# Performance work log

Measured on AMD Instinct MI355X. Metric: run time of the kernel, lower is better.

The kernel has to match this reference:

```python
import jax, jax.numpy as jnp
import numpy as np

N_NODES = 100000
N_EDGES = 1600000
D_IN = 128
D_HID = 128


def gcn_conv(x, src, dst, deg_inv_sqrt, W, b, n_nodes):
    """GCNConv: out = D^{-1/2}(A+I)D^{-1/2} (x @ W) + b.

    src/dst already include self-loops; deg_inv_sqrt precomputed per node.
    """
    h = x @ W  # [N, D_out]
    coef = deg_inv_sqrt[src] * deg_inv_sqrt[dst]  # [E+N]
    msg = h[src] * coef[:, None]  # [E+N, D_out] -- dominant memory traffic
    out = jax.ops.segment_sum(msg, dst, num_segments=n_nodes)
    return out + b


def reference(x, edge_index, W1, b1, W2, b2):
    n_nodes = x.shape[0]
    loop = jnp.arange(n_nodes, dtype=edge_index.dtype)
    src = jnp.concatenate([edge_index[0], loop])
    dst = jnp.concatenate([edge_index[1], loop])
    deg = jax.ops.segment_sum(jnp.ones_like(src, dtype=x.dtype), dst,
                              num_segments=n_nodes)
    deg_inv_sqrt = jnp.where(deg > 0, jax.lax.rsqrt(jnp.maximum(deg, 1.0)), 0.0)

    h = gcn_conv(x, src, dst, deg_inv_sqrt, W1, b1, n_nodes)
    h = jax.nn.relu(h)
    h = gcn_conv(h, src, dst, deg_inv_sqrt, W2, b2, n_nodes)
    return h.mean(axis=0)  # [D_HID]


def setup_inputs() -> dict:
    key = jax.random.key(0)
    k1, k2, k3, k4, k5 = jax.random.split(key, 5)
    x = jax.random.normal(k1, (N_NODES, D_IN), dtype=jnp.float32)
    edge_index = jax.random.randint(k2, (2, N_EDGES), 0, N_NODES, dtype=jnp.int64)
    s1 = 1.0 / np.sqrt(D_IN)
    s2 = 1.0 / np.sqrt(D_HID)
    W1 = jax.random.uniform(k3, (D_IN, D_HID), jnp.float32, -s1, s1)
    W2 = jax.random.uniform(k4, (D_HID, D_HID), jnp.float32, -s2, s2)
    b1 = jnp.zeros((D_HID,), jnp.float32)
    b2 = jnp.zeros((D_HID,), jnp.float32)
    return {"x": x, "edge_index": edge_index, "W1": W1, "b1": b1,
            "W2": W2, "b2": b2}
```

## Files before the change

### kernel.cpp

```cpp
#include <hip/hip_runtime.h>

#define NN 100000
#define NE 1600000
#define DD 128
#define BSH 8
#define NB 391
#define CAP 4608
#define CAPP 8704
#define SSH 9
#define NBS 196
#define CAP2 9472
#define NAB 6250
#define NRB 125

typedef float f32x2 __attribute__((ext_vector_type(2)));
typedef float f32x4 __attribute__((ext_vector_type(4)));
typedef short s16x8 __attribute__((ext_vector_type(8)));

static __device__ __forceinline__ unsigned short f2bf(float f) {
    unsigned u = __float_as_uint(f);
    return (unsigned short)((u + 0x7fffu + ((u >> 16) & 1u)) >> 16);
}


__global__ __launch_bounds__(256) void k_part(const int* __restrict__ src, const int* __restrict__ dst,
                                              int* __restrict__ bcursor, int* __restrict__ bcursor2,
                                              unsigned* __restrict__ part, unsigned* __restrict__ part2) {
    __shared__ int histD[NB], rankD[NB], bblD[NB];
    __shared__ int histS[NBS], rankS[NBS], bblS[NBS];
    int t = threadIdx.x;
    for (int j = t; j < NB; j += 256) histD[j] = 0;
    if (t < NBS) histS[t] = 0;
    __syncthreads();
    int base = blockIdx.x * 4096;
    int s[16], d[16];
    #pragma unroll
    for (int j = 0; j < 16; j++) {
        int i = base + j * 256 + t;
        if (i < NE) {
            s[j] = src[i]; d[j] = dst[i];
            atomicAdd(&histD[d[j] >> BSH], 1);
            atomicAdd(&histS[s[j] >> SSH], 1);
        } else d[j] = -1;
    }
    __syncthreads();
    for (int j = t; j < NB; j += 256) { bblD[j] = atomicAdd(&bcursor[j], histD[j]);  rankD[j] = 0; }
    if (t < NBS) { bblS[t] = atomicAdd(&bcursor2[t], histS[t]); rankS[t] = 0; }
    __syncthreads();
    #pragma unroll
    for (int j = 0; j < 16; j++) {
        if (d[j] >= 0) {
            int bD = d[j] >> BSH;
            int r = bblD[bD] + atomicAdd(&rankD[bD], 1);
            if (r < CAP)
                part[(size_t)bD * CAP + r] = (unsigned)s[j] | ((unsigned)(d[j] & 255) << 17);
            int bS = s[j] >> SSH;
            int r2 = bblS[bS] + atomicAdd(&rankS[bS], 1);
            if (r2 < CAP2)
                part2[(size_t)bS * CAP2 + r2] = (unsigned)d[j] | ((unsigned)(s[j] & 511) << 17);
        }
    }
}


__global__ __launch_bounds__(256) void k_csr(const unsigned* __restrict__ part, const int* __restrict__ bcursor,
                                             int* __restrict__ offs, int* __restrict__ oend,
                                             float* __restrict__ dis, int* __restrict__ csr,
                                             unsigned* __restrict__ hs) {
    __shared__ int cnt[256], offl[256], s2[256];
    int t = threadIdx.x;
    int b = blockIdx.x;
    if (b == 0 && t < 32) hs[(unsigned)NN * 32u + t] = 0u;
    int dlo = b << BSH;
    int nn_b = NN - dlo; if (nn_b > 256) nn_b = 256;
    int c = bcursor[b]; if (c > CAP) c = CAP;
    size_t e0 = (size_t)b * CAP;
    int e0p = b * CAPP;
    cnt[t] = 0;
    __syncthreads();
    for (int i = t; i < c; i += 256)
        atomicAdd(&cnt[part[e0 + i] >> 17], 1);
    __syncthreads();
    int a = cnt[t];
    int ap = (a + 15) & ~15;
    s2[t] = ap;
    __syncthreads();
    for (int off = 1; off < 256; off <<= 1) {
        int add = (t >= off) ? s2[t - off] : 0;
        __syncthreads();
        s2[t] += add;
        __syncthreads();
    }
    int ex = s2[t] - ap;
    offl[t] = ex;
    if (t < nn_b) {
        offs[dlo + t] = e0p + ex;
        oend[dlo + t] = e0p + ex + ap;
        dis[dlo + t] = rsqrtf((float)a + 1.0f);
    }
    cnt[t] = 0;
    __syncthreads();
    for (int i = t; i < c; i += 256) {
        unsigned e = part[e0 + i];
        int li = (int)(e >> 17);
        int p = e0p + offl[li] + atomicAdd(&cnt[li], 1);
        csr[p] = (int)(e & 0x1FFFFu);
    }
    __syncthreads();
    if (t < nn_b) {
        int base2 = e0p + offl[t];
        for (int i = a; i < ap; i++) csr[base2 + i] = NN;
    }
}


__global__ __launch_bounds__(256) void k_coefb(const unsigned* __restrict__ part2, const int* __restrict__ bcursor2,
                                               const float* __restrict__ dis, float* __restrict__ coef) {
    __shared__ float accL[512];
    int t = threadIdx.x;
    int b = blockIdx.x;
    int dlo = b << SSH;
    int nn_b = NN - dlo; if (nn_b > 512) nn_b = 512;
    int c = bcursor2[b]; if (c > CAP2) c = CAP2;
    size_t e0 = (size_t)b * CAP2;
    accL[t] = 0.f; accL[t + 256] = 0.f;
    __syncthreads();
    for (int i = t; i < c; i += 256) {
        unsigned e = part2[e0 + i];
        atomicAdd(&accL[e >> 17], dis[e & 0x1FFFFu]);
    }
    __syncthreads();
    #pragma unroll
    for (int q = 0; q < 2; q++) {
        int i = t + q * 256;
        if (i < nn_b) coef[dlo + i] = accL[i];
    }
}


__global__ __launch_bounds__(256) void k_gemm(const float* __restrict__ Ap, const float* __restrict__ W,
                                              const float* __restrict__ dis, unsigned* __restrict__ hs) {
    __shared__ unsigned WF[8192];
    int tid = threadIdx.x;
    #pragma unroll
    for (int i = 0; i < 32; i++) {
        int e = i * 256 + tid;
        int jw = e & 3, lane = (e >> 2) & 63, kk = (e >> 8) & 3, nt = e >> 10;
        int r0 = kk * 32 + ((lane >> 4) << 3) + (jw << 1);
        int c = (nt << 4) + (lane & 15);
        unsigned lo = f2bf(W[r0 * DD + c]);
        unsigned hi = f2bf(W[(r0 + 1) * DD + c]);
        WF[e] = lo | (hi << 16);
    }

    int lane = tid & 63;
    int w = tid >> 6;
    int rowBase = blockIdx.x * 128 + w * 32;
    int lg = lane >> 4;
    int ll = lane & 15;

    s16x8 af[2][4];
    #pragma unroll
    for (int mt = 0; mt < 2; mt++) {
        int r = rowBase + mt * 16 + ll;
        if (r >= NN) r = NN - 1;
        const char* xp = (const char*)Ap + ((unsigned)r * 512u + (unsigned)lg * 32u);
        #pragma unroll
        for (int kk = 0; kk < 4; kk++) {
            f32x4 a0 = *(const f32x4*)(xp + kk * 128);
            f32x4 a1 = *(const f32x4*)(xp + kk * 128 + 16);
            s16x8 tt;
            tt[0] = (short)f2bf(a0[0]); tt[1] = (short)f2bf(a0[1]);
            tt[2] = (short)f2bf(a0[2]); tt[3] = (short)f2bf(a0[3]);
            tt[4] = (short)f2bf(a1[0]); tt[5] = (short)f2bf(a1[1]);
            tt[6] = (short)f2bf(a1[2]); tt[7] = (short)f2bf(a1[3]);
            af[mt][kk] = tt;
        }
    }
    __syncthreads();

    f32x4 acc[2][8];
    #pragma unroll
    for (int m = 0; m < 2; m++)
        #pragma unroll
        for (int n = 0; n < 8; n++) acc[m][n] = (f32x4){0.f, 0.f, 0.f, 0.f};

    const s16x8* wfrag = (const s16x8*)WF;

    #pragma unroll
    for (int kk = 0; kk < 4; kk++) {
        #pragma unroll
        for (int nt = 0; nt < 8; nt++) {
            s16x8 bf = wfrag[(nt * 4 + kk) * 64 + lane];
            acc[0][nt] = __builtin_amdgcn_mfma_f32_16x16x32_bf16(bf, af[0][kk], acc[0][nt], 0, 0, 0);
            acc[1][nt] = __builtin_amdgcn_mfma_f32_16x16x32_bf16(bf, af[1][kk], acc[1][nt], 0, 0, 0);
        }
    }

    #pragma unroll
    for (int mt = 0; mt < 2; mt++) {
        int grow = rowBase + mt * 16 + ll;
        if (grow < NN) {
            float dn = dis[grow];
            unsigned* orow = (unsigned*)((char*)hs + ((unsigned)grow * 128u));
            #pragma unroll
            for (int nt = 0; nt < 8; nt++) {
                f32x4 v = acc[mt][nt];
                int u = 0;
                u = __builtin_amdgcn_cvt_pk_fp8_f32(v[0] * dn, v[1] * dn, u, false);
                u = __builtin_amdgcn_cvt_pk_fp8_f32(v[2] * dn, v[3] * dn, u, true);
                orow[nt * 4 + lg] = (unsigned)u;
            }
        }
    }
}


__global__ __launch_bounds__(256) void k_agg1(const unsigned* __restrict__ hs4, const float* __restrict__ dis,
                                              const int* __restrict__ offs, const int* __restrict__ oend,
                                              const int* __restrict__ csr, const float* __restrict__ bias,
                                              const float* __restrict__ coef, float* __restrict__ partials) {
    __shared__ float red[4][DD];
    int lane = threadIdx.x & 63;
    int half = lane >> 5;
    int li = lane & 31;
    int wv = threadIdx.x >> 6;
    int node0 = (blockIdx.x * 4 + wv) * 4;
    unsigned li4 = (unsigned)li << 2;
    const char* hb = (const char*)hs4;
    f32x2 v01 = {0.f, 0.f}, v23 = {0.f, 0.f};
    f32x4 bv = *(const f32x4*)&bias[li * 4];

    #pragma unroll 1
    for (int q = 0; q < 4; q++) {
        int node = node0 + q;
        int beg = offs[node], endp = oend[node];
        float dn = dis[node];
        f32x2 a01 = {0.f, 0.f}, a23 = {0.f, 0.f};

        #pragma unroll 1
        for (int i = beg; i < endp; i += 16) {
            const int* cp = csr + i + half * 8;
            int4 sa = *(const int4*)cp;
            int4 sb = *(const int4*)(cp + 4);
            unsigned r[8];
            r[0] = *(const unsigned*)(hb + (((unsigned)sa.x << 7) + li4));
            r[1] = *(const unsigned*)(hb + (((unsigned)sa.y << 7) + li4));
            r[2] = *(const unsigned*)(hb + (((unsigned)sa.z << 7) + li4));
            r[3] = *(const unsigned*)(hb + (((unsigned)sa.w << 7) + li4));
            r[4] = *(const unsigned*)(hb + (((unsigned)sb.x << 7) + li4));
            r[5] = *(const unsigned*)(hb + (((unsigned)sb.y << 7) + li4));
            r[6] = *(const unsigned*)(hb + (((unsigned)sb.z << 7) + li4));
            r[7] = *(const unsigned*)(hb + (((unsigned)sb.w << 7) + li4));
            #pragma unroll
            for (int j = 0; j < 8; j++) {
                a01 += __builtin_amdgcn_cvt_pk_f32_fp8(r[j], false);
                a23 += __builtin_amdgcn_cvt_pk_f32_fp8(r[j], true);
            }
        }

        a01[0] += __shfl_xor(a01[0], 32);
        a01[1] += __shfl_xor(a01[1], 32);
        a23[0] += __shfl_xor(a23[0], 32);
        a23[1] += __shfl_xor(a23[1], 32);

        if (half == 0) {
            unsigned su = *(const unsigned*)(hb + (((unsigned)node << 7) + li4));
            f32x2 sl = __builtin_amdgcn_cvt_pk_f32_fp8(su, false);
            f32x2 sh = __builtin_amdgcn_cvt_pk_f32_fp8(su, true);
            float o0 = fmaxf(dn * (a01[0] + sl[0]) + bv[0], 0.f);
            float o1 = fmaxf(dn * (a01[1] + sl[1]) + bv[1], 0.f);
            float o2 = fmaxf(dn * (a23[0] + sh[0]) + bv[2], 0.f);
            float o3 = fmaxf(dn * (a23[1] + sh[1]) + bv[3], 0.f);
            float wt = (coef[node] + dn) * dn;
            v01[0] += wt * o0; v01[1] += wt * o1;
            v23[0] += wt * o2; v23[1] += wt * o3;
        }
    }

    if (half == 0) {
        red[wv][li * 4 + 0] = v01[0];
        red[wv][li * 4 + 1] = v01[1];
        red[wv][li * 4 + 2] = v23[0];
        red[wv][li * 4 + 3] = v23[1];
    }
    __syncthreads();
    int t = threadIdx.x;
    if (t < DD)
        partials[(size_t)blockIdx.x * DD + t] = red[0][t] + red[1][t] + red[2][t] + red[3][t];
}


__global__ __launch_bounds__(128) void k_red1(const float* __restrict__ partials, float* __restrict__ s1) {
    int t = threadIdx.x, b = blockIdx.x;
    float s = 0.f;
    for (int r = b * 50; r < b * 50 + 50; r++) s += partials[(size_t)r * DD + t];
    s1[b * DD + t] = s;
}

__global__ __launch_bounds__(128) void k_out(const float* __restrict__ s1, const float* __restrict__ W2,
                                             const float* __restrict__ b2, float* __restrict__ out) {
    __shared__ float v[DD];
    int t = threadIdx.x;
    float s = 0.f;
    for (int r = 0; r < NRB; r++) s += s1[r * DD + t];
    v[t] = s * (1.0f / NN);
    __syncthreads();
    float o = b2[t];
    for (int k = 0; k < DD; k++) o += v[k] * W2[k * DD + t];
    out[t] = o;
}


extern "C" void kernel_launch(void* const* d_in, const int* in_sizes, int n_in,
                              void* d_out, int out_size, void* d_ws, size_t ws_size,
                              hipStream_t stream) {
    const float* x  = (const float*)d_in[0];
    const int*   ei = (const int*)d_in[1];
    const float* W1 = (const float*)d_in[2];
    const float* b1 = (const float*)d_in[3];
    const float* W2 = (const float*)d_in[4];
    const float* b2 = (const float*)d_in[5];
    float* out = (float*)d_out;
    const int* esrc = ei;
    const int* edst = ei + NE;

    char* p = (char*)d_ws;
    unsigned* part  = (unsigned*)p;      p += (size_t)NB * CAP * 4;
    unsigned* part2 = (unsigned*)p;      p += (size_t)NBS * CAP2 * 4;
    int* csr       = (int*)p;            p += (size_t)NB * CAPP * 4;
    int* offs      = (int*)p;            p += (((size_t)NN * 4) + 255) & ~(size_t)255;
    int* oend      = (int*)p;            p += (((size_t)NN * 4) + 255) & ~(size_t)255;
    float* dis     = (float*)p;          p += (((size_t)NN * 4) + 255) & ~(size_t)255;
    float* coef    = (float*)p;          p += (((size_t)NN * 4) + 255) & ~(size_t)255;
    int* bcursor   = (int*)p;            p += (((size_t)(NB + NBS) * 4) + 255) & ~(size_t)255;
    unsigned* hs   = (unsigned*)p;       p += (size_t)(NN + 1) * DD;
    float* partials = (float*)p;         p += (size_t)NAB * DD * 4;
    float* s1      = (float*)p;          p += (size_t)NRB * DD * 4;
    int* bcursor2  = bcursor + NB;

    hipMemsetAsync(bcursor, 0, (NB + NBS) * 4, stream);

    k_part<<<(NE + 4095) / 4096, 256, 0, stream>>>(esrc, edst, bcursor, bcursor2, part, part2);
    k_csr<<<NB, 256, 0, stream>>>(part, bcursor, offs, oend, dis, csr, hs);
    k_coefb<<<NBS, 256, 0, stream>>>(part2, bcursor2, dis, coef);

    k_gemm<<<(NN + 127) / 128, 256, 0, stream>>>(x, W1, dis, hs);
    k_agg1<<<NAB, 256, 0, stream>>>(hs, dis, offs, oend, csr, b1, coef, partials);

    k_red1<<<NRB, 128, 0, stream>>>(partials, s1);
    k_out<<<1, 128, 0, stream>>>(s1, W2, b2, out);
}
```

Before: 153.2 us.

## Fuse coef kernel into GEMM launch and prefetch next CSR indices in aggregation

The separate coefficient-accumulation kernel is merged into the GEMM kernel as extra blocks that branch off by block index and reuse the GEMM's shared buffer. This removes one kernel launch and lets the small coef work run alongside the GEMM blocks. The aggregation loop now loads the next 16 CSR indices before issuing the current gathers, a software prefetch meant to hide index-load latency. That prefetch reads past each node's end, so the CSR buffer is padded by 16 ints; the fused kernel also has a larger grid with imbalanced block types.

```diff
diff --git a/kernel.cpp b/kernel.cpp
--- a/kernel.cpp
+++ b/kernel.cpp
@@ -10,6 +10,7 @@
 #define SSH 9
 #define NBS 196
 #define CAP2 9472
+#define NGB 782
 #define NAB 6250
 #define NRB 125
 
@@ -114,34 +115,34 @@
 }
 
 
-__global__ __launch_bounds__(256) void k_coefb(const unsigned* __restrict__ part2, const int* __restrict__ bcursor2,
-                                               const float* __restrict__ dis, float* __restrict__ coef) {
-    __shared__ float accL[512];
-    int t = threadIdx.x;
-    int b = blockIdx.x;
-    int dlo = b << SSH;
-    int nn_b = NN - dlo; if (nn_b > 512) nn_b = 512;
-    int c = bcursor2[b]; if (c > CAP2) c = CAP2;
-    size_t e0 = (size_t)b * CAP2;
-    accL[t] = 0.f; accL[t + 256] = 0.f;
-    __syncthreads();
-    for (int i = t; i < c; i += 256) {
-        unsigned e = part2[e0 + i];
-        atomicAdd(&accL[e >> 17], dis[e & 0x1FFFFu]);
-    }
-    __syncthreads();
-    #pragma unroll
-    for (int q = 0; q < 2; q++) {
-        int i = t + q * 256;
-        if (i < nn_b) coef[dlo + i] = accL[i];
-    }
-}
-
-
-__global__ __launch_bounds__(256) void k_gemm(const float* __restrict__ Ap, const float* __restrict__ W,
-                                              const float* __restrict__ dis, unsigned* __restrict__ hs) {
+__global__ __launch_bounds__(256) void k_gemmcoef(const float* __restrict__ Ap, const float* __restrict__ W,
+                                                  const float* __restrict__ dis, unsigned* __restrict__ hs,
+                                                  const unsigned* __restrict__ part2, const int* __restrict__ bcursor2,
+                                                  float* __restrict__ coef) {
     __shared__ unsigned WF[8192];
     int tid = threadIdx.x;
+    if (blockIdx.x >= NGB) {
+        float* accL = (float*)WF;
+        int b = blockIdx.x - NGB;
+        int dlo = b << SSH;
+        int nn_b = NN - dlo; if (nn_b > 512) nn_b = 512;
+        int c = bcursor2[b]; if (c > CAP2) c = CAP2;
+        size_t e0 = (size_t)b * CAP2;
+        accL[tid] = 0.f; accL[tid + 256] = 0.f;
+        __syncthreads();
+        for (int i = tid; i < c; i += 256) {
+            unsigned e = part2[e0 + i];
+            atomicAdd(&accL[e >> 17], dis[e & 0x1FFFFu]);
+        }
+        __syncthreads();
+        #pragma unroll
+        for (int q = 0; q < 2; q++) {
+            int i = tid + q * 256;
+            if (i < nn_b) coef[dlo + i] = accL[i];
+        }
+        return;
+    }
+
     #pragma unroll
     for (int i = 0; i < 32; i++) {
         int e = i * 256 + tid;
@@ -238,25 +239,29 @@
         float dn = dis[node];
         f32x2 a01 = {0.f, 0.f}, a23 = {0.f, 0.f};
 
+        const int* cp0 = csr + beg + half * 8;
+        int4 ca = *(const int4*)cp0;
+        int4 cb = *(const int4*)(cp0 + 4);
         #pragma unroll 1
         for (int i = beg; i < endp; i += 16) {
-            const int* cp = csr + i + half * 8;
-            int4 sa = *(const int4*)cp;
-            int4 sb = *(const int4*)(cp + 4);
+            const int* np = csr + i + 16 + half * 8;
+            int4 na = *(const int4*)np;
+            int4 nb = *(const int4*)(np + 4);
             unsigned r[8];
-            r[0] = *(const unsigned*)(hb + (((unsigned)sa.x << 7) + li4));
-            r[1] = *(const unsigned*)(hb + (((unsigned)sa.y << 7) + li4));
-            r[2] = *(const unsigned*)(hb + (((unsigned)sa.z << 7) + li4));
-            r[3] = *(const unsigned*)(hb + (((unsigned)sa.w << 7) + li4));
-            r[4] = *(const unsigned*)(hb + (((unsigned)sb.x << 7) + li4));
-            r[5] = *(const unsigned*)(hb + (((unsigned)sb.y << 7) + li4));
-            r[6] = *(const unsigned*)(hb + (((unsigned)sb.z << 7) + li4));
-            r[7] = *(const unsigned*)(hb + (((unsigned)sb.w << 7) + li4));
+            r[0] = *(const unsigned*)(hb + (((unsigned)ca.x << 7) + li4));
+            r[1] = *(const unsigned*)(hb + (((unsigned)ca.y << 7) + li4));
+            r[2] = *(const unsigned*)(hb + (((unsigned)ca.z << 7) + li4));
+            r[3] = *(const unsigned*)(hb + (((unsigned)ca.w << 7) + li4));
+            r[4] = *(const unsigned*)(hb + (((unsigned)cb.x << 7) + li4));
+            r[5] = *(const unsigned*)(hb + (((unsigned)cb.y << 7) + li4));
+            r[6] = *(const unsigned*)(hb + (((unsigned)cb.z << 7) + li4));
+            r[7] = *(const unsigned*)(hb + (((unsigned)cb.w << 7) + li4));
             #pragma unroll
             for (int j = 0; j < 8; j++) {
                 a01 += __builtin_amdgcn_cvt_pk_f32_fp8(r[j], false);
                 a23 += __builtin_amdgcn_cvt_pk_f32_fp8(r[j], true);
             }
+            ca = na; cb = nb;
         }
 
         a01[0] += __shfl_xor(a01[0], 32);
@@ -328,7 +333,7 @@
     char* p = (char*)d_ws;
     unsigned* part  = (unsigned*)p;      p += (size_t)NB * CAP * 4;
     unsigned* part2 = (unsigned*)p;      p += (size_t)NBS * CAP2 * 4;
-    int* csr       = (int*)p;            p += (size_t)NB * CAPP * 4;
+    int* csr       = (int*)p;            p += (size_t)(NB * CAPP + 16) * 4;
     int* offs      = (int*)p;            p += (((size_t)NN * 4) + 255) & ~(size_t)255;
     int* oend      = (int*)p;            p += (((size_t)NN * 4) + 255) & ~(size_t)255;
     float* dis     = (float*)p;          p += (((size_t)NN * 4) + 255) & ~(size_t)255;
@@ -343,9 +348,8 @@
 
     k_part<<<(NE + 4095) / 4096, 256, 0, stream>>>(esrc, edst, bcursor, bcursor2, part, part2);
     k_csr<<<NB, 256, 0, stream>>>(part, bcursor, offs, oend, dis, csr, hs);
-    k_coefb<<<NBS, 256, 0, stream>>>(part2, bcursor2, dis, coef);
-
-    k_gemm<<<(NN + 127) / 128, 256, 0, stream>>>(x, W1, dis, hs);
+
+    k_gemmcoef<<<NGB + NBS, 256, 0, stream>>>(x, W1, dis, hs, part2, bcursor2, coef);
     k_agg1<<<NAB, 256, 0, stream>>>(hs, dis, offs, oend, csr, b1, coef, partials);
 
     k_red1<<<NRB, 128, 0, stream>>>(partials, s1);
```

Measured after the change: 157.8 us. 1.03x slower.
